# Optimization experiments

Measured on AMD Instinct MI355X. Metric: run time of the kernel, lower is better.

The kernel has to match this reference:

```python
import jax, jax.numpy as jnp
import numpy as np

NC_MEM = 64          # nTemporalMemoryChannels
NC_IMG = 64          # nImageFeatureChannels
FTL_RATIO = 0.5      # temporalFTLRatio
N_BLOCKS = 3         # nTemporalBlocks
B, H, W = 32, 64, 96
M = 32               # memory buffer length (= max(memory_idx)+1)


def setup_inputs() -> dict:
    key = jax.random.key(0)
    ks = jax.random.split(key, 8)
    eye = jnp.eye(4, dtype=jnp.float32)
    img_features = jax.random.normal(ks[0], (B, NC_IMG, H, W), jnp.float32)
    prev_mem_features = jax.random.normal(ks[1], (M, NC_MEM, H, W), jnp.float32)
    # extrinsics: random perturbation around identity so torch.inverse-equivalent is well conditioned
    prev_extrinsics = 0.1 * jax.random.normal(ks[2], (M, 4, 4), jnp.float32) + eye
    cur_extrinsics = 0.1 * jax.random.normal(ks[3], (B, 4, 4), jnp.float32) + eye
    memory_idx = jnp.arange(B, dtype=jnp.int32)
    use_memory = jax.random.randint(ks[4], (B,), 0, 2).astype(bool)
    NC = NC_MEM + NC_IMG
    Ws = jax.random.normal(ks[5], (N_BLOCKS, NC, NC), jnp.float32) * (1.0 / np.sqrt(NC))
    bs = jax.random.normal(ks[6], (N_BLOCKS, NC), jnp.float32) * 0.01
    return {
        "img_features": img_features,
        "prev_mem_features": prev_mem_features,
        "prev_extrinsics": prev_extrinsics,
        "cur_extrinsics": cur_extrinsics,
        "memory_idx": memory_idx,
        "use_memory": use_memory,
        "Ws": Ws,
        "bs": bs,
    }


def _apply_ftl(xf, feats, ratio):
    # Feature Transform Layer: first `ratio` fraction of channels (rounded down
    # to a multiple of 4) treated as groups of homogeneous 4-vectors per pixel,
    # warped by the 4x4 transform xf; remaining channels pass through.
    b, c, h, w = feats.shape
    nc_ftl = (int(c * ratio) // 4) * 4
    g = nc_ftl // 4
    pts = feats[:, :nc_ftl].reshape(b, g, 4, h * w)
    pts = jnp.einsum("bij,bgjp->bgip", xf, pts).reshape(b, nc_ftl, h, w)
    return jnp.concatenate([pts, feats[:, nc_ftl:]], axis=1)


def reference(img_features, prev_mem_features, prev_extrinsics, cur_extrinsics,
              memory_idx, use_memory, Ws, bs):
    eye = jnp.eye(4, dtype=prev_extrinsics.dtype)
    # --- transform_memory_features (gather + extrinsics warp, masked) ---
    mem_g = prev_mem_features[memory_idx]              # [B, NC_MEM, H, W]
    prev_ext_g = prev_extrinsics[memory_idx]           # [B, 4, 4]
    # entries with use_memory=False are zeroed; guard inverse with identity
    safe_prev = jnp.where(use_memory[:, None, None], prev_ext_g, eye)
    prev_cam0_to_world = jnp.linalg.inv(safe_prev)
    xf = jnp.einsum("bij,bjk->bik", cur_extrinsics, prev_cam0_to_world)
    mem_xfed = _apply_ftl(xf, mem_g, FTL_RATIO)
    mem_xfed = jnp.where(use_memory[:, None, None, None], mem_xfed,
                         jnp.zeros((), mem_xfed.dtype))
    # --- forward_one_step: concat + 1x1 conv stack (pointwise matmuls) ---
    x = jnp.concatenate([mem_xfed, img_features], axis=1)  # [B, 128, H, W]
    n = Ws.shape[0]
    for i in range(n):
        x = jnp.einsum("oc,bchw->bohw", Ws[i], x) + bs[i][None, :, None, None]
        if i != n - 1:
            x = jax.nn.relu(x)
    fused_features = x[:, NC_MEM:]                     # returned output
    return fused_features
```

## Files before the change

kernel.cpp:

```cpp
#include <hip/hip_runtime.h>

#define NC_MEM 64
#define NC_IMG 64
#define NC     128
#define B_     32
#define H_     64
#define W_     96
#define HW_    (H_ * W_)
#define P_TILE 64
#define NTILES (HW_ / P_TILE)
#define RS     144

#define WA_HI  0
#define WA_LO  98304
#define XF_OFF 196608
#define UM_OFF 198656

typedef __attribute__((ext_vector_type(8))) short bf16x8;
typedef __attribute__((ext_vector_type(4))) float f32x4;

__device__ inline unsigned short f2bf(float x) {
    unsigned u = __float_as_uint(x);
    return (unsigned short)((u + 0x7FFFu + ((u >> 16) & 1u)) >> 16);
}
__device__ inline float bf2f(unsigned short h) {
    return __uint_as_float(((unsigned)h) << 16);
}

__global__ void prep_xf(const float* __restrict__ prev_ext,
                        const float* __restrict__ cur_ext,
                        const int* __restrict__ mem_idx,
                        const unsigned char* __restrict__ um_raw,
                        unsigned char* __restrict__ wsb) {
    int b = threadIdx.x;
    if (b >= B_) return;

    bool is_bool = false;
    for (int i = 0; i < 32; ++i)
        if ((i & 3) && um_raw[i]) is_bool = true;
    bool um = is_bool ? (um_raw[b] != 0) : (((const int*)um_raw)[b] != 0);

    int mi = mem_idx[b];
    float A[4][4], inv[4][4];
    for (int i = 0; i < 4; ++i)
        for (int j = 0; j < 4; ++j) {
            A[i][j]   = um ? prev_ext[mi * 16 + i * 4 + j] : (i == j ? 1.f : 0.f);
            inv[i][j] = (i == j) ? 1.f : 0.f;
        }
    for (int col = 0; col < 4; ++col) {
        int piv = col; float best = fabsf(A[col][col]);
        for (int r = col + 1; r < 4; ++r) {
            float v = fabsf(A[r][col]);
            if (v > best) { best = v; piv = r; }
        }
        if (piv != col)
            for (int j = 0; j < 4; ++j) {
                float t = A[col][j]; A[col][j] = A[piv][j]; A[piv][j] = t;
                t = inv[col][j]; inv[col][j] = inv[piv][j]; inv[piv][j] = t;
            }
        float d = 1.0f / A[col][col];
        for (int j = 0; j < 4; ++j) { A[col][j] *= d; inv[col][j] *= d; }
        for (int r = 0; r < 4; ++r) {
            if (r == col) continue;
            float f = A[r][col];
            for (int j = 0; j < 4; ++j) {
                A[r][j] -= f * A[col][j];
                inv[r][j] -= f * inv[col][j];
            }
        }
    }
    float* xf = (float*)(wsb + XF_OFF) + b * 16;
    for (int i = 0; i < 4; ++i)
        for (int j = 0; j < 4; ++j) {
            float s = 0.f;
            for (int k = 0; k < 4; ++k)
                s += cur_ext[b * 16 + i * 4 + k] * inv[k][j];
            xf[i * 4 + j] = s;
        }
    ((float*)(wsb + UM_OFF))[b] = um ? 1.f : 0.f;
}

__global__ void prep_w(const float* __restrict__ Ws, unsigned char* __restrict__ wsb) {
    int idx = blockIdx.x * 256 + threadIdx.x;
    if (idx >= 3 * NC * NC) return;
    int l = idx >> 14, r = idx & 16383, o = r >> 7, c = r & 127;
    float w = Ws[idx];
    unsigned short hi = f2bf(w);
    unsigned short lo = f2bf(w - bf2f(hi));
    int mt = o >> 4, lm = o & 15, ks = c >> 5, kr = c & 31, q = kr >> 3, j = kr & 7;
    int lane = q * 16 + lm;
    int di = ((((l * 8 + mt) * 4 + ks) * 64 + lane) << 3) + j;
    ((unsigned short*)(wsb + WA_HI))[di] = hi;
    ((unsigned short*)(wsb + WA_LO))[di] = lo;
}

__global__ __launch_bounds__(256)
void fused_main(const float* __restrict__ img, const float* __restrict__ mem,
                const int* __restrict__ mem_idx, const float* __restrict__ bs,
                const unsigned char* __restrict__ wsb, float* __restrict__ out) {
    __shared__ unsigned short xh[64 * RS];
    __shared__ unsigned short xl[64 * RS];

    const int t   = threadIdx.x;
    const int b   = blockIdx.y;
    const int hw0 = blockIdx.x * P_TILE;
    const bool umb = ((const float*)(wsb + UM_OFF))[b] != 0.f;
    const int mi  = mem_idx[b];

    const bf16x8* __restrict__ WH = (const bf16x8*)(wsb + WA_HI);
    const bf16x8* __restrict__ WL = (const bf16x8*)(wsb + WA_LO);

    {
        const int px = t & 63, cq = t >> 6;
        float xfv[16];
        if (umb) {
            const float* xfp = (const float*)(wsb + XF_OFF) + b * 16;
#pragma unroll
            for (int i = 0; i < 16; ++i) xfv[i] = xfp[i];
        }
        const int pstart = umb ? 0 : 4;
        for (int p = pstart; p < 8; ++p) {
            int gg = p * 4 + cq;
            int c0 = gg * 4;
            const float* src = (c0 < 64)
                ? (mem + ((size_t)mi * 64 + c0) * HW_ + hw0 + px)
                : (img + ((size_t)b  * 64 + (c0 - 64)) * HW_ + hw0 + px);
            float v[4];
            v[0] = src[0]; v[1] = src[HW_]; v[2] = src[2 * HW_]; v[3] = src[3 * HW_];
            if (umb && gg < 8) {
                float r0 = xfv[0]  * v[0] + xfv[1]  * v[1] + xfv[2]  * v[2] + xfv[3]  * v[3];
                float r1 = xfv[4]  * v[0] + xfv[5]  * v[1] + xfv[6]  * v[2] + xfv[7]  * v[3];
                float r2 = xfv[8]  * v[0] + xfv[9]  * v[1] + xfv[10] * v[2] + xfv[11] * v[3];
                float r3 = xfv[12] * v[0] + xfv[13] * v[1] + xfv[14] * v[2] + xfv[15] * v[3];
                v[0] = r0; v[1] = r1; v[2] = r2; v[3] = r3;
            }
            unsigned hs[4], ls[4];
#pragma unroll
            for (int i = 0; i < 4; ++i) {
                hs[i] = f2bf(v[i]);
                ls[i] = f2bf(v[i] - bf2f((unsigned short)hs[i]));
            }
            uint2 hp = make_uint2(hs[0] | (hs[1] << 16), hs[2] | (hs[3] << 16));
            uint2 lp = make_uint2(ls[0] | (ls[1] << 16), ls[2] | (ls[3] << 16));
            *(uint2*)&xh[px * RS + c0] = hp;
            *(uint2*)&xl[px * RS + c0] = lp;
        }
    }
    __syncthreads();

    const int w    = t >> 6;
    const int lane = t & 63;
    const int q    = lane >> 4;
    const int lm   = lane & 15;

    const int mt0 = 2 * w;
#pragma unroll
    for (int l = 0; l < 2; ++l) {
        f32x4 acc[2][4];
#pragma unroll
        for (int mi2 = 0; mi2 < 2; ++mi2) {
            f32x4 bv = *(const f32x4*)&bs[l * NC + (mt0 + mi2) * 16 + q * 4];
#pragma unroll
            for (int nt = 0; nt < 4; ++nt) acc[mi2][nt] = bv;
        }
        const int ks0 = (l == 0 && !umb) ? 2 : 0;
        for (int ks = ks0; ks < 4; ++ks) {
            int f0 = ((l * 8 + mt0) * 4 + ks) * 64 + lane;
            int f1 = ((l * 8 + mt0 + 1) * 4 + ks) * 64 + lane;
            bf16x8 ah0 = WH[f0], al0 = WL[f0];
            bf16x8 ah1 = WH[f1], al1 = WL[f1];
#pragma unroll
            for (int nt = 0; nt < 4; ++nt) {
                bf16x8 bh = *(const bf16x8*)&xh[(nt * 16 + lm) * RS + ks * 32 + q * 8];
                bf16x8 bl = *(const bf16x8*)&xl[(nt * 16 + lm) * RS + ks * 32 + q * 8];
                acc[0][nt] = __builtin_amdgcn_mfma_f32_16x16x32_bf16(ah0, bh, acc[0][nt], 0, 0, 0);
                acc[1][nt] = __builtin_amdgcn_mfma_f32_16x16x32_bf16(ah1, bh, acc[1][nt], 0, 0, 0);
                acc[0][nt] = __builtin_amdgcn_mfma_f32_16x16x32_bf16(al0, bh, acc[0][nt], 0, 0, 0);
                acc[1][nt] = __builtin_amdgcn_mfma_f32_16x16x32_bf16(al1, bh, acc[1][nt], 0, 0, 0);
                acc[0][nt] = __builtin_amdgcn_mfma_f32_16x16x32_bf16(ah0, bl, acc[0][nt], 0, 0, 0);
                acc[1][nt] = __builtin_amdgcn_mfma_f32_16x16x32_bf16(ah1, bl, acc[1][nt], 0, 0, 0);
            }
        }
        __syncthreads();
#pragma unroll
        for (int mi2 = 0; mi2 < 2; ++mi2) {
            int o0 = (mt0 + mi2) * 16 + q * 4;
#pragma unroll
            for (int nt = 0; nt < 4; ++nt) {
                int ppx = nt * 16 + lm;
                unsigned hs[4], ls[4];
#pragma unroll
                for (int r = 0; r < 4; ++r) {
                    float v = fmaxf(acc[mi2][nt][r], 0.f);
                    hs[r] = f2bf(v);
                    ls[r] = f2bf(v - bf2f((unsigned short)hs[r]));
                }
                *(uint2*)&xh[ppx * RS + o0] = make_uint2(hs[0] | (hs[1] << 16), hs[2] | (hs[3] << 16));
                *(uint2*)&xl[ppx * RS + o0] = make_uint2(ls[0] | (ls[1] << 16), ls[2] | (ls[3] << 16));
            }
        }
        __syncthreads();
    }

    {
        const int mt2 = 4 + w;
        f32x4 acc[4];
        f32x4 bv = *(const f32x4*)&bs[2 * NC + mt2 * 16 + q * 4];
#pragma unroll
        for (int nt = 0; nt < 4; ++nt) acc[nt] = bv;
#pragma unroll
        for (int ks = 0; ks < 4; ++ks) {
            int f = ((2 * 8 + mt2) * 4 + ks) * 64 + lane;
            bf16x8 ah = WH[f], al = WL[f];
#pragma unroll
            for (int nt = 0; nt < 4; ++nt) {
                bf16x8 bh = *(const bf16x8*)&xh[(nt * 16 + lm) * RS + ks * 32 + q * 8];
                bf16x8 bl = *(const bf16x8*)&xl[(nt * 16 + lm) * RS + ks * 32 + q * 8];
                acc[nt] = __builtin_amdgcn_mfma_f32_16x16x32_bf16(ah, bh, acc[nt], 0, 0, 0);
                acc[nt] = __builtin_amdgcn_mfma_f32_16x16x32_bf16(al, bh, acc[nt], 0, 0, 0);
                acc[nt] = __builtin_amdgcn_mfma_f32_16x16x32_bf16(ah, bl, acc[nt], 0, 0, 0);
            }
        }
        const int oc0 = mt2 * 16 + q * 4 - 64;
#pragma unroll
        for (int nt = 0; nt < 4; ++nt) {
            float* dst = out + ((size_t)b * 64 + oc0) * HW_ + hw0 + nt * 16 + lm;
#pragma unroll
            for (int r = 0; r < 4; ++r)
                dst[(size_t)r * HW_] = acc[nt][r];
        }
    }
}

extern "C" void kernel_launch(void* const* d_in, const int* in_sizes, int n_in,
                              void* d_out, int out_size, void* d_ws, size_t ws_size,
                              hipStream_t stream) {
    const float* img  = (const float*)d_in[0];
    const float* mem  = (const float*)d_in[1];
    const float* pext = (const float*)d_in[2];
    const float* cext = (const float*)d_in[3];
    const int*   midx = (const int*)d_in[4];
    const unsigned char* umem = (const unsigned char*)d_in[5];
    const float* Ws   = (const float*)d_in[6];
    const float* bs   = (const float*)d_in[7];
    float* out = (float*)d_out;
    unsigned char* wsb = (unsigned char*)d_ws;

    hipLaunchKernelGGL(prep_xf, dim3(1), dim3(64), 0, stream, pext, cext, midx, umem, wsb);
    hipLaunchKernelGGL(prep_w, dim3(192), dim3(256), 0, stream, Ws, wsb);
    hipLaunchKernelGGL(fused_main, dim3(NTILES, B_), dim3(256), 0, stream,
                       img, mem, midx, bs, wsb, out);
}
```

Baseline: 184.0 us.

## Merge prep kernels, truncate bf16 split, shrink LDS stride, raise occupancy

Merges the weight-packing and extrinsics-inverse kernels into one launch, and replaces Gauss-Jordan elimination with a closed-form cofactor 4x4 inverse. In the main kernel, the hi/lo bf16 split of activations now uses truncation plus byte-permute instead of round-to-nearest, which lowers ALU cost while keeping hi+lo nearly exact. The LDS row stride drops from 144 to 136 to cut shared memory use and change the bank pattern. Launch bounds now request 4 blocks per SM, and the K-step loop is unrolled by hand. Risks are register pressure from the occupancy hint and possible bank conflicts at the new stride.

```diff
diff --git a/kernel.cpp b/kernel.cpp
--- a/kernel.cpp
+++ b/kernel.cpp
@@ -9,7 +9,7 @@
 #define HW_    (H_ * W_)
 #define P_TILE 64
 #define NTILES (HW_ / P_TILE)
-#define RS     144
+#define RS     136
 
 #define WA_HI  0
 #define WA_LO  98304
@@ -19,7 +19,7 @@
 typedef __attribute__((ext_vector_type(8))) short bf16x8;
 typedef __attribute__((ext_vector_type(4))) float f32x4;
 
-__device__ inline unsigned short f2bf(float x) {
+__device__ inline unsigned short f2bf_rn(float x) {
     unsigned u = __float_as_uint(x);
     return (unsigned short)((u + 0x7FFFu + ((u >> 16) & 1u)) >> 16);
 }
@@ -27,11 +27,25 @@
     return __uint_as_float(((unsigned)h) << 16);
 }
 
-__global__ void prep_xf(const float* __restrict__ prev_ext,
-                        const float* __restrict__ cur_ext,
-                        const int* __restrict__ mem_idx,
-                        const unsigned char* __restrict__ um_raw,
-                        unsigned char* __restrict__ wsb) {
+__global__ void prep(const float* __restrict__ Ws,
+                     const float* __restrict__ prev_ext,
+                     const float* __restrict__ cur_ext,
+                     const int* __restrict__ mem_idx,
+                     const unsigned char* __restrict__ um_raw,
+                     unsigned char* __restrict__ wsb) {
+    if (blockIdx.x < 192) {
+        int idx = blockIdx.x * 256 + threadIdx.x;
+        int l = idx >> 14, r = idx & 16383, o = r >> 7, c = r & 127;
+        float w = Ws[idx];
+        unsigned short hi = f2bf_rn(w);
+        unsigned short lo = f2bf_rn(w - bf2f(hi));
+        int mt = o >> 4, lm = o & 15, ks = c >> 5, kr = c & 31, q = kr >> 3, j = kr & 7;
+        int lane = q * 16 + lm;
+        int di = ((((l * 8 + mt) * 4 + ks) * 64 + lane) << 3) + j;
+        ((unsigned short*)(wsb + WA_HI))[di] = hi;
+        ((unsigned short*)(wsb + WA_LO))[di] = lo;
+        return;
+    }
     int b = threadIdx.x;
     if (b >= B_) return;
 
@@ -39,62 +53,61 @@
     for (int i = 0; i < 32; ++i)
         if ((i & 3) && um_raw[i]) is_bool = true;
     bool um = is_bool ? (um_raw[b] != 0) : (((const int*)um_raw)[b] != 0);
-
     int mi = mem_idx[b];
-    float A[4][4], inv[4][4];
+
+    float a[16];
+#pragma unroll
+    for (int i = 0; i < 16; ++i)
+        a[i] = um ? prev_ext[mi * 16 + i] : ((i % 5 == 0) ? 1.f : 0.f);
+
+    float s0 = a[0]*a[5]  - a[1]*a[4];
+    float s1 = a[0]*a[6]  - a[2]*a[4];
+    float s2 = a[0]*a[7]  - a[3]*a[4];
+    float s3 = a[1]*a[6]  - a[2]*a[5];
+    float s4 = a[1]*a[7]  - a[3]*a[5];
+    float s5 = a[2]*a[7]  - a[3]*a[6];
+    float c5 = a[10]*a[15] - a[11]*a[14];
+    float c4 = a[9]*a[15]  - a[11]*a[13];
+    float c3 = a[9]*a[14]  - a[10]*a[13];
+    float c2 = a[8]*a[15]  - a[11]*a[12];
+    float c1 = a[8]*a[14]  - a[10]*a[12];
+    float c0 = a[8]*a[13]  - a[9]*a[12];
+    float det = s0*c5 - s1*c4 + s2*c3 + s3*c2 - s4*c1 + s5*c0;
+    float id = 1.0f / det;
+
+    float inv[16];
+    inv[0]  = ( a[5]*c5  - a[6]*c4  + a[7]*c3)  * id;
+    inv[1]  = (-a[1]*c5  + a[2]*c4  - a[3]*c3)  * id;
+    inv[2]  = ( a[13]*s5 - a[14]*s4 + a[15]*s3) * id;
+    inv[3]  = (-a[9]*s5  + a[10]*s4 - a[11]*s3) * id;
+    inv[4]  = (-a[4]*c5  + a[6]*c2  - a[7]*c1)  * id;
+    inv[5]  = ( a[0]*c5  - a[2]*c2  + a[3]*c1)  * id;
+    inv[6]  = (-a[12]*s5 + a[14]*s2 - a[15]*s1) * id;
+    inv[7]  = ( a[8]*s5  - a[10]*s2 + a[11]*s1) * id;
+    inv[8]  = ( a[4]*c4  - a[5]*c2  + a[7]*c0)  * id;
+    inv[9]  = (-a[0]*c4  + a[1]*c2  - a[3]*c0)  * id;
+    inv[10] = ( a[12]*s4 - a[13]*s2 + a[15]*s0) * id;
+    inv[11] = (-a[8]*s4  + a[9]*s2  - a[11]*s0) * id;
+    inv[12] = (-a[4]*c3  + a[5]*c1  - a[6]*c0)  * id;
+    inv[13] = ( a[0]*c3  - a[1]*c1  + a[2]*c0)  * id;
+    inv[14] = (-a[12]*s3 + a[13]*s1 - a[14]*s0) * id;
+    inv[15] = ( a[8]*s3  - a[9]*s1  + a[10]*s0) * id;
+
+    float* xf = (float*)(wsb + XF_OFF) + b * 16;
+#pragma unroll
     for (int i = 0; i < 4; ++i)
-        for (int j = 0; j < 4; ++j) {
-            A[i][j]   = um ? prev_ext[mi * 16 + i * 4 + j] : (i == j ? 1.f : 0.f);
-            inv[i][j] = (i == j) ? 1.f : 0.f;
-        }
-    for (int col = 0; col < 4; ++col) {
-        int piv = col; float best = fabsf(A[col][col]);
-        for (int r = col + 1; r < 4; ++r) {
-            float v = fabsf(A[r][col]);
-            if (v > best) { best = v; piv = r; }
-        }
-        if (piv != col)
-            for (int j = 0; j < 4; ++j) {
-                float t = A[col][j]; A[col][j] = A[piv][j]; A[piv][j] = t;
-                t = inv[col][j]; inv[col][j] = inv[piv][j]; inv[piv][j] = t;
-            }
-        float d = 1.0f / A[col][col];
-        for (int j = 0; j < 4; ++j) { A[col][j] *= d; inv[col][j] *= d; }
-        for (int r = 0; r < 4; ++r) {
-            if (r == col) continue;
-            float f = A[r][col];
-            for (int j = 0; j < 4; ++j) {
-                A[r][j] -= f * A[col][j];
-                inv[r][j] -= f * inv[col][j];
-            }
-        }
-    }
-    float* xf = (float*)(wsb + XF_OFF) + b * 16;
-    for (int i = 0; i < 4; ++i)
-        for (int j = 0; j < 4; ++j) {
+#pragma unroll
+        for (int j2 = 0; j2 < 4; ++j2) {
             float s = 0.f;
+#pragma unroll
             for (int k = 0; k < 4; ++k)
-                s += cur_ext[b * 16 + i * 4 + k] * inv[k][j];
-            xf[i * 4 + j] = s;
+                s += cur_ext[b * 16 + i * 4 + k] * inv[k * 4 + j2];
+            xf[i * 4 + j2] = s;
         }
     ((float*)(wsb + UM_OFF))[b] = um ? 1.f : 0.f;
 }
 
-__global__ void prep_w(const float* __restrict__ Ws, unsigned char* __restrict__ wsb) {
-    int idx = blockIdx.x * 256 + threadIdx.x;
-    if (idx >= 3 * NC * NC) return;
-    int l = idx >> 14, r = idx & 16383, o = r >> 7, c = r & 127;
-    float w = Ws[idx];
-    unsigned short hi = f2bf(w);
-    unsigned short lo = f2bf(w - bf2f(hi));
-    int mt = o >> 4, lm = o & 15, ks = c >> 5, kr = c & 31, q = kr >> 3, j = kr & 7;
-    int lane = q * 16 + lm;
-    int di = ((((l * 8 + mt) * 4 + ks) * 64 + lane) << 3) + j;
-    ((unsigned short*)(wsb + WA_HI))[di] = hi;
-    ((unsigned short*)(wsb + WA_LO))[di] = lo;
-}
-
-__global__ __launch_bounds__(256)
+__global__ __launch_bounds__(256, 4)
 void fused_main(const float* __restrict__ img, const float* __restrict__ mem,
                 const int* __restrict__ mem_idx, const float* __restrict__ bs,
                 const unsigned char* __restrict__ wsb, float* __restrict__ out) {
@@ -125,23 +138,24 @@
             const float* src = (c0 < 64)
                 ? (mem + ((size_t)mi * 64 + c0) * HW_ + hw0 + px)
                 : (img + ((size_t)b  * 64 + (c0 - 64)) * HW_ + hw0 + px);
-            float v[4];
-            v[0] = src[0]; v[1] = src[HW_]; v[2] = src[2 * HW_]; v[3] = src[3 * HW_];
+            float v0 = src[0], v1 = src[HW_], v2 = src[2 * HW_], v3 = src[3 * HW_];
             if (umb && gg < 8) {
-                float r0 = xfv[0]  * v[0] + xfv[1]  * v[1] + xfv[2]  * v[2] + xfv[3]  * v[3];
-                float r1 = xfv[4]  * v[0] + xfv[5]  * v[1] + xfv[6]  * v[2] + xfv[7]  * v[3];
-                float r2 = xfv[8]  * v[0] + xfv[9]  * v[1] + xfv[10] * v[2] + xfv[11] * v[3];
-                float r3 = xfv[12] * v[0] + xfv[13] * v[1] + xfv[14] * v[2] + xfv[15] * v[3];
-                v[0] = r0; v[1] = r1; v[2] = r2; v[3] = r3;
-            }
-            unsigned hs[4], ls[4];
-#pragma unroll
-            for (int i = 0; i < 4; ++i) {
-                hs[i] = f2bf(v[i]);
-                ls[i] = f2bf(v[i] - bf2f((unsigned short)hs[i]));
-            }
-            uint2 hp = make_uint2(hs[0] | (hs[1] << 16), hs[2] | (hs[3] << 16));
-            uint2 lp = make_uint2(ls[0] | (ls[1] << 16), ls[2] | (ls[3] << 16));
+                float r0 = xfv[0]  * v0 + xfv[1]  * v1 + xfv[2]  * v2 + xfv[3]  * v3;
+                float r1 = xfv[4]  * v0 + xfv[5]  * v1 + xfv[6]  * v2 + xfv[7]  * v3;
+                float r2 = xfv[8]  * v0 + xfv[9]  * v1 + xfv[10] * v2 + xfv[11] * v3;
+                float r3 = xfv[12] * v0 + xfv[13] * v1 + xfv[14] * v2 + xfv[15] * v3;
+                v0 = r0; v1 = r1; v2 = r2; v3 = r3;
+            }
+            unsigned u0 = __float_as_uint(v0), u1 = __float_as_uint(v1);
+            unsigned u2 = __float_as_uint(v2), u3 = __float_as_uint(v3);
+            unsigned l0 = __float_as_uint(v0 - __uint_as_float(u0 & 0xFFFF0000u));
+            unsigned l1 = __float_as_uint(v1 - __uint_as_float(u1 & 0xFFFF0000u));
+            unsigned l2 = __float_as_uint(v2 - __uint_as_float(u2 & 0xFFFF0000u));
+            unsigned l3 = __float_as_uint(v3 - __uint_as_float(u3 & 0xFFFF0000u));
+            uint2 hp = make_uint2(__builtin_amdgcn_perm(u1, u0, 0x07060302u),
+                                  __builtin_amdgcn_perm(u3, u2, 0x07060302u));
+            uint2 lp = make_uint2(__builtin_amdgcn_perm(l1, l0, 0x07060302u),
+                                  __builtin_amdgcn_perm(l3, l2, 0x07060302u));
             *(uint2*)&xh[px * RS + c0] = hp;
             *(uint2*)&xl[px * RS + c0] = lp;
         }
@@ -163,8 +177,7 @@
 #pragma unroll
             for (int nt = 0; nt < 4; ++nt) acc[mi2][nt] = bv;
         }
-        const int ks0 = (l == 0 && !umb) ? 2 : 0;
-        for (int ks = ks0; ks < 4; ++ks) {
+        auto do_ks = [&](int ks) {
             int f0 = ((l * 8 + mt0) * 4 + ks) * 64 + lane;
             int f1 = ((l * 8 + mt0 + 1) * 4 + ks) * 64 + lane;
             bf16x8 ah0 = WH[f0], al0 = WL[f0];
@@ -180,7 +193,10 @@
                 acc[0][nt] = __builtin_amdgcn_mfma_f32_16x16x32_bf16(ah0, bl, acc[0][nt], 0, 0, 0);
                 acc[1][nt] = __builtin_amdgcn_mfma_f32_16x16x32_bf16(ah1, bl, acc[1][nt], 0, 0, 0);
             }
-        }
+        };
+        if (l == 0 && !umb) { do_ks(2); do_ks(3); }
+        else { do_ks(0); do_ks(1); do_ks(2); do_ks(3); }
+
         __syncthreads();
 #pragma unroll
         for (int mi2 = 0; mi2 < 2; ++mi2) {
@@ -188,15 +204,22 @@
 #pragma unroll
             for (int nt = 0; nt < 4; ++nt) {
                 int ppx = nt * 16 + lm;
-                unsigned hs[4], ls[4];
-#pragma unroll
-                for (int r = 0; r < 4; ++r) {
-                    float v = fmaxf(acc[mi2][nt][r], 0.f);
-                    hs[r] = f2bf(v);
-                    ls[r] = f2bf(v - bf2f((unsigned short)hs[r]));
-                }
-                *(uint2*)&xh[ppx * RS + o0] = make_uint2(hs[0] | (hs[1] << 16), hs[2] | (hs[3] << 16));
-                *(uint2*)&xl[ppx * RS + o0] = make_uint2(ls[0] | (ls[1] << 16), ls[2] | (ls[3] << 16));
+                float v0 = fmaxf(acc[mi2][nt][0], 0.f);
+                float v1 = fmaxf(acc[mi2][nt][1], 0.f);
+                float v2 = fmaxf(acc[mi2][nt][2], 0.f);
+                float v3 = fmaxf(acc[mi2][nt][3], 0.f);
+                unsigned u0 = __float_as_uint(v0), u1 = __float_as_uint(v1);
+                unsigned u2 = __float_as_uint(v2), u3 = __float_as_uint(v3);
+                unsigned l0 = __float_as_uint(v0 - __uint_as_float(u0 & 0xFFFF0000u));
+                unsigned l1 = __float_as_uint(v1 - __uint_as_float(u1 & 0xFFFF0000u));
+                unsigned l2 = __float_as_uint(v2 - __uint_as_float(u2 & 0xFFFF0000u));
+                unsigned l3 = __float_as_uint(v3 - __uint_as_float(u3 & 0xFFFF0000u));
+                *(uint2*)&xh[ppx * RS + o0] =
+                    make_uint2(__builtin_amdgcn_perm(u1, u0, 0x07060302u),
+                               __builtin_amdgcn_perm(u3, u2, 0x07060302u));
+                *(uint2*)&xl[ppx * RS + o0] =
+                    make_uint2(__builtin_amdgcn_perm(l1, l0, 0x07060302u),
+                               __builtin_amdgcn_perm(l3, l2, 0x07060302u));
             }
         }
         __syncthreads();
@@ -246,8 +269,8 @@
     float* out = (float*)d_out;
     unsigned char* wsb = (unsigned char*)d_ws;
 
-    hipLaunchKernelGGL(prep_xf, dim3(1), dim3(64), 0, stream, pext, cext, midx, umem, wsb);
-    hipLaunchKernelGGL(prep_w, dim3(192), dim3(256), 0, stream, Ws, wsb);
+    hipLaunchKernelGGL(prep, dim3(193), dim3(256), 0, stream,
+                       Ws, pext, cext, midx, umem, wsb);
     hipLaunchKernelGGL(fused_main, dim3(NTILES, B_), dim3(256), 0, stream,
                        img, mem, midx, bs, wsb, out);
 }
```

Result: faster. 175.9 us (-4.4%).
